# Kernel optimization log

Hardware: AMD Instinct MI355X
Metric: run time of the kernel (lower is better)

The kernel has to match this reference:

```python
import jax, jax.numpy as jnp
import numpy as np

PATCH = 16      # sqrt(n_patches=256)
ALPHA = 10.0
HEADS, DH = 2, 64


def _fourier(coords, Bm):
    # coords: (HW, 2), Bm: (n_features, 2) -> (HW, 2*n_features)
    proj = 2.0 * jnp.pi * coords @ Bm.T
    return jnp.concatenate([jnp.cos(proj), jnp.sin(proj)], axis=-1)


def _forward(coords_decoding, tokens, B_q, B_l0, B_l1,
             qW, qb, toqW, tokvW, tooW, toob,
             bwW0, bwb0, bwW1, bwb1,
             modW0, modb0, modW1, modb1,
             hvW0, hvb0, outW0, outb0, outW1, outb1):
    B = coords_decoding.shape[0]
    Hh, Ww = coords_decoding.shape[1], coords_decoding.shape[2]
    coords = coords_decoding.reshape(B, -1, coords_decoding.shape[-1])
    grid = coords[0]                      # (HW, 2); coords_modulation is None -> same grid
    HW = grid.shape[0]
    m = tokens.shape[1]

    # patch indices and spatial bias
    row = jnp.clip((grid[:, 0] * PATCH).astype(jnp.int32), 0, PATCH - 1)
    col = jnp.clip((grid[:, 1] * PATCH).astype(jnp.int32), 0, PATCH - 1)
    idx = row * PATCH + col               # (HW,)
    t = idx.astype(jnp.float32) / (PATCH * PATCH)
    pos = (jnp.arange(m, dtype=jnp.float32) + 0.5) / m
    rel = -ALPHA * jnp.abs(t[None, :] - pos[:, None]) ** 2   # (m, HW)
    bias = rel.T                          # (HW, m), broadcast over batch & heads

    # query features (shared across batch)
    xq = jax.nn.relu(_fourier(grid, B_q) @ qW + qb)           # (HW, hd)
    xq_b = jnp.broadcast_to(xq[None], (B, HW, xq.shape[-1]))

    # cross attention with spatial bias
    q = (xq_b @ toqW).reshape(B, HW, HEADS, DH).transpose(0, 2, 1, 3)   # (B,h,HW,Dh)
    kv = tokens @ tokvW                                                  # (B,m,2*inner)
    k, v = jnp.split(kv, 2, axis=-1)
    k = k.reshape(B, m, HEADS, DH).transpose(0, 2, 1, 3)                 # (B,h,m,Dh)
    v = v.reshape(B, m, HEADS, DH).transpose(0, 2, 1, 3)
    sim = jnp.einsum('bhqd,bhkd->bhqk', q, k) * (DH ** -0.5) + bias[None, None]
    attn = jax.nn.softmax(sim, axis=-1)
    o = jnp.einsum('bhqk,bhkd->bhqd', attn, v)
    o = o.transpose(0, 2, 1, 3).reshape(B, HW, HEADS * DH)
    mod = o @ tooW + toob                                                # (B,HW,hd)

    # per-band MLP stack (layer_num = 2)
    def band(Bl, bwW, bwb, mW, mb):
        h = jax.nn.relu(_fourier(grid, Bl) @ bwW + bwb)                  # (HW,hd)
        return jax.nn.relu(h[None] + mod @ mW + mb)                      # (B,HW,hd)

    m0 = band(B_l0, bwW0, bwb0, modW0, modb0)
    m1 = band(B_l1, bwW1, bwb1, modW1, modb1)
    hv0 = m0
    hv1 = jax.nn.relu((m1 + hv0) @ hvW0 + hvb0)
    out = (hv0 @ outW0 + outb0) + (hv1 @ outW1 + outb1)                  # (B,HW,3)
    return out.reshape(B, Hh, Ww, -1)


def setup_inputs() -> dict:
    key = jax.random.key(0)
    ks = jax.random.split(key, 32)
    B, H, W, L = 4, 128, 128, 256
    fd, hd, cd, od = 64, 256, 256, 3
    nf = fd // 2
    inner = HEADS * DH

    def lin(k, i, o):
        return jax.random.normal(k, (i, o), dtype=jnp.float32) / np.sqrt(i).astype(np.float32)

    inp = {}
    inp['coords_decoding'] = jax.random.uniform(ks[0], (B, H, W, 2), dtype=jnp.float32)
    inp['tokens'] = jax.random.normal(ks[1], (B, L, cd), dtype=jnp.float32)
    inp['B_q'] = jax.random.normal(ks[2], (nf, 2), dtype=jnp.float32) / 16.0
    inp['B_l0'] = jax.random.normal(ks[3], (nf, 2), dtype=jnp.float32) / 128.0
    inp['B_l1'] = jax.random.normal(ks[4], (nf, 2), dtype=jnp.float32) / 32.0
    inp['qW'] = lin(ks[5], fd, hd); inp['qb'] = jnp.zeros((hd,), jnp.float32)
    inp['toqW'] = lin(ks[6], hd, inner)
    inp['tokvW'] = lin(ks[7], cd, inner * 2)
    inp['tooW'] = lin(ks[8], inner, hd); inp['toob'] = jnp.zeros((hd,), jnp.float32)
    inp['bwW0'] = lin(ks[9], fd, hd); inp['bwb0'] = jnp.zeros((hd,), jnp.float32)
    inp['bwW1'] = lin(ks[10], fd, hd); inp['bwb1'] = jnp.zeros((hd,), jnp.float32)
    inp['modW0'] = lin(ks[11], hd, hd); inp['modb0'] = jnp.zeros((hd,), jnp.float32)
    inp['modW1'] = lin(ks[12], hd, hd); inp['modb1'] = jnp.zeros((hd,), jnp.float32)
    inp['hvW0'] = lin(ks[13], hd, hd); inp['hvb0'] = jnp.zeros((hd,), jnp.float32)
    inp['outW0'] = lin(ks[14], hd, od); inp['outb0'] = jnp.zeros((od,), jnp.float32)
    inp['outW1'] = lin(ks[15], hd, od); inp['outb1'] = jnp.zeros((od,), jnp.float32)
    return inp


def reference(coords_decoding, tokens, B_q, B_l0, B_l1,
              qW, qb, toqW, tokvW, tooW, toob,
              bwW0, bwb0, bwW1, bwb1,
              modW0, modb0, modW1, modb1,
              hvW0, hvb0, outW0, outb0, outW1, outb1):
    return _forward(coords_decoding, tokens, B_q, B_l0, B_l1,
                    qW, qb, toqW, tokvW, tooW, toob,
                    bwW0, bwb0, bwW1, bwb1,
                    modW0, modb0, modW1, modb1,
                    hvW0, hvb0, outW0, outb0, outW1, outb1)
```

## Files before the change

kernel.cpp:

```cpp
#include <hip/hip_runtime.h>
#include <stdint.h>

constexpr int kHW = 16384;
constexpr int kB  = 4;
constexpr int kM  = 256;

typedef _Float16 half8 __attribute__((ext_vector_type(8)));
typedef __attribute__((ext_vector_type(4))) float f32x4;
typedef unsigned int u32x4 __attribute__((ext_vector_type(4)));

__device__ __forceinline__ unsigned short f2h(float f) {
  _Float16 h = (_Float16)f;
  return __builtin_bit_cast(unsigned short, h);
}
__device__ __forceinline__ float h2f(unsigned short u) {
  return (float)__builtin_bit_cast(_Float16, u);
}

__global__ __launch_bounds__(256) void wprep_kernel(
    const float* __restrict__ tooW, const float* __restrict__ modW0,
    const float* __restrict__ modW1, const float* __restrict__ hvW0,
    const float* __restrict__ qW, const float* __restrict__ bwW0,
    const float* __restrict__ bwW1, const float* __restrict__ toqW,
    unsigned short* __restrict__ tooWt, unsigned short* __restrict__ modW0t,
    unsigned short* __restrict__ modW1t, unsigned short* __restrict__ hvW0t,
    unsigned short* __restrict__ qWt, unsigned short* __restrict__ bw0t,
    unsigned short* __restrict__ bw1t, unsigned short* __restrict__ toqWt)
{
  int m = blockIdx.x, tid = threadIdx.x;
  const float* Ws[8] = {tooW, modW0, modW1, hvW0, qW, bwW0, bwW1, toqW};
  unsigned short* Wts[8] = {tooWt, modW0t, modW1t, hvW0t, qWt, bw0t, bw1t, toqWt};
  const int Ks[8] = {128, 256, 256, 256, 64, 64, 64, 256};
  const int Ns[8] = {256, 256, 256, 256, 256, 256, 256, 128};
  const float* W = Ws[m];
  unsigned short* Wt = Wts[m];
  int K = Ks[m], N = Ns[m];
  if (tid < N) {
    for (int kb = 0; kb < K / 8; kb++) {
      unsigned short sv[8];
#pragma unroll
      for (int i = 0; i < 8; i++)
        sv[i] = f2h(W[(kb * 8 + i) * N + tid]);
      *(uint4*)&Wt[tid * K + kb * 8] = *(const uint4*)sv;
    }
  }
}

__global__ __launch_bounds__(256) void kv_kernel(
    const float* __restrict__ tokens, const float* __restrict__ tokvW,
    unsigned short* __restrict__ kn_ws, unsigned short* __restrict__ vt_ws)
{
  __shared__ __align__(16) float tok[256];
  int b = blockIdx.y, j = blockIdx.x, c = threadIdx.x;
  tok[c] = tokens[(b * kM + j) * 256 + c];
  __syncthreads();
  float acc = 0.f;
  for (int i4 = 0; i4 < 64; i4++) {
    float4 t4 = *(const float4*)&tok[i4 * 4];
    acc += t4.x * tokvW[(i4*4+0)*256 + c] + t4.y * tokvW[(i4*4+1)*256 + c]
         + t4.z * tokvW[(i4*4+2)*256 + c] + t4.w * tokvW[(i4*4+3)*256 + c];
  }
  unsigned short hv = f2h(acc);
  if (c < 128) {
    int h = c >> 6, dd = c & 63;
    kn_ws[((size_t)(b*2+h)*256 + j) * 64 + dd] = hv;
  } else {
    int c2 = c - 128;
    int h = c2 >> 6, dd = c2 & 63;
    vt_ws[((size_t)(b*2+h)*64 + dd) * 256 + j] = hv;
  }
}

constexpr int kFPitch = 72;
constexpr int kXPitch = 264;

__global__ __launch_bounds__(256, 2) void feat_kernel(
    const float* __restrict__ coords,
    const float* __restrict__ Bq, const float* __restrict__ Bl0, const float* __restrict__ Bl1,
    const float* __restrict__ qb, const float* __restrict__ bwb0, const float* __restrict__ bwb1,
    const unsigned short* __restrict__ qWt, const unsigned short* __restrict__ bw0t,
    const unsigned short* __restrict__ bw1t, const unsigned short* __restrict__ toqWt,
    float* __restrict__ t_ws, unsigned short* __restrict__ qc_ws,
    unsigned short* __restrict__ h0_hf, unsigned short* __restrict__ h1_hf)
{
  __shared__ __align__(16) unsigned short ff_s[3][32][kFPitch];
  __shared__ __align__(16) unsigned short xq_s[32][kXPitch];
  __shared__ float coords_s[64];

  int tid = threadIdx.x;
  int px0 = blockIdx.x * 32;
  int w = tid >> 6, ln = tid & 63;
  int c = ln & 15, q = ln >> 4;

  if (tid < 64) coords_s[tid] = coords[px0 * 2 + tid];
  __syncthreads();

#pragma unroll
  for (int r = 0; r < 24; r++) {
    int v = r * 256 + tid;
    int mat = v >> 11;
    int p = (v >> 6) & 31;
    int f = v & 63;
    int fr = f & 31;
    const float* Bm = (mat == 0) ? Bq : (mat == 1 ? Bl0 : Bl1);
    float x = coords_s[p * 2 + 0];
    float y = coords_s[p * 2 + 1];
    float proj = 6.283185307179586f * (x * Bm[fr*2+0] + y * Bm[fr*2+1]);
    float s, cc;
    __sincosf(proj, &s, &cc);
    ff_s[mat][p][f] = f2h((f < 32) ? cc : s);
  }
  if (tid < 32) {
    float x = coords_s[tid * 2 + 0];
    float y = coords_s[tid * 2 + 1];
    int row = min(max((int)(x * 16.0f), 0), 15);
    int col = min(max((int)(y * 16.0f), 0), 15);
    t_ws[px0 + tid] = (float)(row * 16 + col) * (1.0f / 256.0f);
  }
  __syncthreads();

  const f32x4 zero4 = {0.f, 0.f, 0.f, 0.f};

  for (int mat = 0; mat < 3; mat++) {
    const unsigned short* Wt = (mat == 0) ? qWt : (mat == 1 ? bw0t : bw1t);
    const float* bias = (mat == 0) ? qb : (mat == 1 ? bwb0 : bwb1);
    f32x4 acc[8];
#pragma unroll
    for (int i = 0; i < 8; i++) acc[i] = zero4;
#pragma unroll
    for (int ks = 0; ks < 2; ks++) {
      int koff = ks * 32 + q * 8;
      half8 bfr[4];
#pragma unroll
      for (int nt = 0; nt < 4; nt++)
        bfr[nt] = *(const half8*)(Wt + (size_t)(w*64 + nt*16 + c) * 64 + koff);
      half8 afr[2];
#pragma unroll
      for (int mt = 0; mt < 2; mt++)
        afr[mt] = *(const half8*)(&ff_s[mat][mt*16 + c][koff]);
#pragma unroll
      for (int mt = 0; mt < 2; mt++)
#pragma unroll
        for (int nt = 0; nt < 4; nt++)
          acc[mt*4+nt] = __builtin_amdgcn_mfma_f32_16x16x32_f16(afr[mt], bfr[nt], acc[mt*4+nt], 0, 0, 0);
    }
    float bv[4];
#pragma unroll
    for (int nt = 0; nt < 4; nt++) bv[nt] = bias[w*64 + nt*16 + c];
#pragma unroll
    for (int mt = 0; mt < 2; mt++)
#pragma unroll
      for (int nt = 0; nt < 4; nt++)
#pragma unroll
        for (int rg = 0; rg < 4; rg++) {
          int row = mt*16 + q*4 + rg, col = w*64 + nt*16 + c;
          unsigned short hv = f2h(fmaxf(acc[mt*4+nt][rg] + bv[nt], 0.f));
          if (mat == 0)      xq_s[row][col] = hv;
          else if (mat == 1) h0_hf[((size_t)(px0 + row)) * 256 + col] = hv;
          else               h1_hf[((size_t)(px0 + row)) * 256 + col] = hv;
        }
  }
  __syncthreads();

  {
    f32x4 acc2[4];
#pragma unroll
    for (int i = 0; i < 4; i++) acc2[i] = zero4;
#pragma unroll
    for (int kt = 0; kt < 8; kt++) {
      int koff = kt * 32 + q * 8;
      half8 bfr[2];
#pragma unroll
      for (int nt = 0; nt < 2; nt++)
        bfr[nt] = *(const half8*)(toqWt + (size_t)(w*32 + nt*16 + c) * 256 + koff);
      half8 afr[2];
#pragma unroll
      for (int mt = 0; mt < 2; mt++)
        afr[mt] = *(const half8*)(&xq_s[mt*16 + c][koff]);
#pragma unroll
      for (int mt = 0; mt < 2; mt++)
#pragma unroll
        for (int nt = 0; nt < 2; nt++)
          acc2[mt*2+nt] = __builtin_amdgcn_mfma_f32_16x16x32_f16(afr[mt], bfr[nt], acc2[mt*2+nt], 0, 0, 0);
    }
#pragma unroll
    for (int mt = 0; mt < 2; mt++)
#pragma unroll
      for (int nt = 0; nt < 2; nt++)
#pragma unroll
        for (int rg = 0; rg < 4; rg++) {
          int row = mt*16 + q*4 + rg, col = w*32 + nt*16 + c;
          qc_ws[((size_t)(px0 + row)) * 128 + col] = f2h(acc2[mt*2+nt][rg]);
        }
  }
}

constexpr int kPPitch = 264;

__global__ __launch_bounds__(256, 2) void attn_kernel(
    const unsigned short* __restrict__ kn_ws,
    const unsigned short* __restrict__ vt_ws,
    const unsigned short* __restrict__ qc_ws,
    const float* __restrict__ t_ws,
    unsigned short* __restrict__ o_hf)
{
  __shared__ __align__(16) unsigned short P_s[32 * kPPitch];
  __shared__ float t_s[32];
  __shared__ float red_max[32][4];
  __shared__ float red_sum[32][4];

  int b = blockIdx.y;
  int px0 = blockIdx.x * 32;
  int tid = threadIdx.x;
  int w = tid >> 6, ln = tid & 63;
  int c = ln & 15, q = ln >> 4;

  if (tid < 32) t_s[tid] = t_ws[px0 + tid];

  const f32x4 zero4 = {0.f, 0.f, 0.f, 0.f};

  for (int h = 0; h < 2; h++) {
    __syncthreads();

    f32x4 acc[8];
#pragma unroll
    for (int i = 0; i < 8; i++) acc[i] = zero4;
    const unsigned short* kbase = kn_ws + (size_t)(b*2+h) * 256 * 64;
#pragma unroll
    for (int ks = 0; ks < 2; ks++) {
      int koff = ks * 32 + q * 8;
      half8 a0 = *(const half8*)(qc_ws + (size_t)(px0 + c) * 128 + h*64 + koff);
      half8 a1 = *(const half8*)(qc_ws + (size_t)(px0 + 16 + c) * 128 + h*64 + koff);
#pragma unroll
      for (int nt = 0; nt < 4; nt++) {
        half8 bf = *(const half8*)(kbase + (size_t)(w*64 + nt*16 + c) * 64 + koff);
        acc[0*4+nt] = __builtin_amdgcn_mfma_f32_16x16x32_f16(a0, bf, acc[0*4+nt], 0, 0, 0);
        acc[1*4+nt] = __builtin_amdgcn_mfma_f32_16x16x32_f16(a1, bf, acc[1*4+nt], 0, 0, 0);
      }
    }

    float lm[2][4];
#pragma unroll
    for (int mt = 0; mt < 2; mt++)
#pragma unroll
      for (int rg = 0; rg < 4; rg++) {
        int row = mt*16 + q*4 + rg;
        float tv = t_s[row];
        float mx = -1e30f;
#pragma unroll
        for (int nt = 0; nt < 4; nt++) {
          int token = w*64 + nt*16 + c;
          float pos = ((float)token + 0.5f) * (1.0f / 256.0f);
          float db = tv - pos;
          float sb = acc[mt*4+nt][rg] * 0.125f - 10.0f * db * db;
          acc[mt*4+nt][rg] = sb;
          mx = fmaxf(mx, sb);
        }
        lm[mt][rg] = mx;
      }
#pragma unroll
    for (int s = 1; s < 16; s <<= 1)
#pragma unroll
      for (int mt = 0; mt < 2; mt++)
#pragma unroll
        for (int rg = 0; rg < 4; rg++)
          lm[mt][rg] = fmaxf(lm[mt][rg], __shfl_xor(lm[mt][rg], s, 64));
    if (c == 0) {
#pragma unroll
      for (int mt = 0; mt < 2; mt++)
#pragma unroll
        for (int rg = 0; rg < 4; rg++)
          red_max[mt*16 + q*4 + rg][w] = lm[mt][rg];
    }
    __syncthreads();

    float ps[2][4];
#pragma unroll
    for (int mt = 0; mt < 2; mt++)
#pragma unroll
      for (int rg = 0; rg < 4; rg++) {
        int row = mt*16 + q*4 + rg;
        float gm = fmaxf(fmaxf(red_max[row][0], red_max[row][1]),
                         fmaxf(red_max[row][2], red_max[row][3]));
        float sum = 0.f;
#pragma unroll
        for (int nt = 0; nt < 4; nt++) {
          float e = __expf(acc[mt*4+nt][rg] - gm);
          sum += e;
          P_s[row * kPPitch + w*64 + nt*16 + c] = f2h(e);
        }
        ps[mt][rg] = sum;
      }
#pragma unroll
    for (int s = 1; s < 16; s <<= 1)
#pragma unroll
      for (int mt = 0; mt < 2; mt++)
#pragma unroll
        for (int rg = 0; rg < 4; rg++)
          ps[mt][rg] += __shfl_xor(ps[mt][rg], s, 64);
    if (c == 0) {
#pragma unroll
      for (int mt = 0; mt < 2; mt++)
#pragma unroll
        for (int rg = 0; rg < 4; rg++)
          red_sum[mt*16 + q*4 + rg][w] = ps[mt][rg];
    }
    __syncthreads();

    f32x4 oacc[2] = {zero4, zero4};
    const unsigned short* vbase = vt_ws + (size_t)(b*2+h) * 64 * 256;
#pragma unroll
    for (int kt = 0; kt < 8; kt++) {
      int koff = kt * 32 + q * 8;
      half8 bf = *(const half8*)(vbase + (size_t)(w*16 + c) * 256 + koff);
      half8 a0 = *(const half8*)(P_s + (0*16 + c) * kPPitch + koff);
      half8 a1 = *(const half8*)(P_s + (1*16 + c) * kPPitch + koff);
      oacc[0] = __builtin_amdgcn_mfma_f32_16x16x32_f16(a0, bf, oacc[0], 0, 0, 0);
      oacc[1] = __builtin_amdgcn_mfma_f32_16x16x32_f16(a1, bf, oacc[1], 0, 0, 0);
    }
#pragma unroll
    for (int mt = 0; mt < 2; mt++)
#pragma unroll
      for (int rg = 0; rg < 4; rg++) {
        int row = mt*16 + q*4 + rg;
        float rinv = 1.0f / (red_sum[row][0] + red_sum[row][1] +
                             red_sum[row][2] + red_sum[row][3]);
        o_hf[((size_t)(b * kHW + px0 + row)) * 128 + h*64 + w*16 + c] =
            f2h(oacc[mt][rg] * rinv);
      }
  }
}

constexpr int kPitch = 264;

template <int KD>
__device__ __forceinline__ void gemm4(
    const unsigned short* abuf, const unsigned short* wt,
    f32x4* acc , int c, int q)
{
  constexpr int NKS = KD / 32;
  const unsigned short* wr0 = wt + (0 * 16 + c) * KD + q * 8;
  const unsigned short* wr1 = wt + (1 * 16 + c) * KD + q * 8;
  const unsigned short* wr2 = wt + (2 * 16 + c) * KD + q * 8;
  const unsigned short* wr3 = wt + (3 * 16 + c) * KD + q * 8;
  half8 bfr[3][4];
#pragma unroll
  for (int p = 0; p < 2; p++) {
    bfr[p][0] = *(const half8*)(wr0 + p * 32);
    bfr[p][1] = *(const half8*)(wr1 + p * 32);
    bfr[p][2] = *(const half8*)(wr2 + p * 32);
    bfr[p][3] = *(const half8*)(wr3 + p * 32);
  }
#pragma unroll
  for (int ks = 0; ks < NKS; ks++) {
    if (ks + 2 < NKS) {
      int slot = (ks + 2) % 3, koff2 = (ks + 2) * 32;
      bfr[slot][0] = *(const half8*)(wr0 + koff2);
      bfr[slot][1] = *(const half8*)(wr1 + koff2);
      bfr[slot][2] = *(const half8*)(wr2 + koff2);
      bfr[slot][3] = *(const half8*)(wr3 + koff2);
    }
    half8 afr[4];
    int koff = ks * 32 + q * 8;
#pragma unroll
    for (int mt = 0; mt < 4; mt++)
      afr[mt] = *(const half8*)(abuf + (mt * 16 + c) * kPitch + koff);
    int cur = ks % 3;
#pragma unroll
    for (int mt = 0; mt < 4; mt++)
#pragma unroll
      for (int nt = 0; nt < 4; nt++)
        acc[mt * 4 + nt] = __builtin_amdgcn_mfma_f32_16x16x32_f16(afr[mt], bfr[cur][nt], acc[mt * 4 + nt], 0, 0, 0);
  }
}

__global__ __launch_bounds__(256, 2) void mlp_kernel(
    const unsigned short* __restrict__ o_hf,
    const unsigned short* __restrict__ h0_hf, const unsigned short* __restrict__ h1_hf,
    const unsigned short* __restrict__ tooWt, const float* __restrict__ toob,
    const unsigned short* __restrict__ modW0t, const float* __restrict__ modb0,
    const unsigned short* __restrict__ modW1t, const float* __restrict__ modb1,
    const unsigned short* __restrict__ hvW0t, const float* __restrict__ hvb0,
    const float* __restrict__ outW0, const float* __restrict__ outb0,
    const float* __restrict__ outW1, const float* __restrict__ outb1,
    float* __restrict__ dout)
{
  __shared__ __align__(16) unsigned short buf0[64 * kPitch];
  __shared__ __align__(16) unsigned short buf1[64 * kPitch];
  __shared__ float scratch[64 * 12];

  int tid = threadIdx.x;
  int px0 = blockIdx.x * 16;
  int w = tid >> 6, ln = tid & 63;
  int c = ln & 15, q = ln >> 4;

  unsigned short h0r[4][4], h1r[4][4];
#pragma unroll
  for (int nt = 0; nt < 4; nt++) {
    int col = w * 64 + nt * 16 + c;
#pragma unroll
    for (int rg = 0; rg < 4; rg++) {
      int px = q * 4 + rg;
      h0r[nt][rg] = __builtin_nontemporal_load(h0_hf + ((size_t)(px0 + px)) * 256 + col);
      h1r[nt][rg] = __builtin_nontemporal_load(h1_hf + ((size_t)(px0 + px)) * 256 + col);
    }
  }

#pragma unroll
  for (int i = 0; i < 4; i++) {
    int idx = i * 256 + tid;
    int r = idx >> 4, c8 = (idx & 15) * 8;
    int b = r >> 4, px = r & 15;
    u32x4 v = __builtin_nontemporal_load(
        (const u32x4*)(o_hf + ((size_t)(b * kHW + px0 + px)) * 128 + c8));
    *(u32x4*)&buf0[r * kPitch + c8] = v;
  }
  __syncthreads();

  const f32x4 zero4 = {0.f, 0.f, 0.f, 0.f};
  f32x4 acc[16];

#pragma unroll
  for (int i = 0; i < 16; i++) acc[i] = zero4;
  gemm4<128>(buf0, tooWt + (size_t)w * 64 * 128, acc, c, q);
  {
    float bias[4];
#pragma unroll
    for (int nt = 0; nt < 4; nt++) bias[nt] = toob[w * 64 + nt * 16 + c];
#pragma unroll
    for (int mt = 0; mt < 4; mt++)
#pragma unroll
      for (int nt = 0; nt < 4; nt++)
#pragma unroll
        for (int rg = 0; rg < 4; rg++) {
          int row = mt * 16 + q * 4 + rg, col = w * 64 + nt * 16 + c;
          buf1[row * kPitch + col] = f2h(acc[mt * 4 + nt][rg] + bias[nt]);
        }
  }
  __syncthreads();

#pragma unroll
  for (int i = 0; i < 16; i++) acc[i] = zero4;
  gemm4<256>(buf1, modW0t + (size_t)w * 64 * 256, acc, c, q);
  {
    float bias[4];
#pragma unroll
    for (int nt = 0; nt < 4; nt++) bias[nt] = modb0[w * 64 + nt * 16 + c];
#pragma unroll
    for (int mt = 0; mt < 4; mt++)
#pragma unroll
      for (int nt = 0; nt < 4; nt++)
#pragma unroll
        for (int rg = 0; rg < 4; rg++) {
          int row = mt * 16 + q * 4 + rg, col = w * 64 + nt * 16 + c;
          buf0[row * kPitch + col] =
              f2h(fmaxf(acc[mt * 4 + nt][rg] + bias[nt] + h2f(h0r[nt][rg]), 0.f));
        }
  }
  __syncthreads();

#pragma unroll
  for (int i = 0; i < 16; i++) acc[i] = zero4;
  gemm4<256>(buf1, modW1t + (size_t)w * 64 * 256, acc, c, q);
  __syncthreads();
  {
    float bias[4];
#pragma unroll
    for (int nt = 0; nt < 4; nt++) bias[nt] = modb1[w * 64 + nt * 16 + c];
#pragma unroll
    for (int mt = 0; mt < 4; mt++)
#pragma unroll
      for (int nt = 0; nt < 4; nt++)
#pragma unroll
        for (int rg = 0; rg < 4; rg++) {
          int row = mt * 16 + q * 4 + rg, col = w * 64 + nt * 16 + c;
          float m0v = h2f(buf0[row * kPitch + col]);
          float v = m0v + fmaxf(acc[mt * 4 + nt][rg] + bias[nt] + h2f(h1r[nt][rg]), 0.f);
          buf1[row * kPitch + col] = f2h(v);
        }
  }
  __syncthreads();

#pragma unroll
  for (int i = 0; i < 16; i++) acc[i] = zero4;
  gemm4<256>(buf1, hvW0t + (size_t)w * 64 * 256, acc, c, q);
  {
    float bias[4], w0v[4][3], w1v[4][3];
#pragma unroll
    for (int nt = 0; nt < 4; nt++) {
      int col = w * 64 + nt * 16 + c;
      bias[nt] = hvb0[col];
#pragma unroll
      for (int k = 0; k < 3; k++) {
        w0v[nt][k] = outW0[col * 3 + k];
        w1v[nt][k] = outW1[col * 3 + k];
      }
    }
#pragma unroll
    for (int mt = 0; mt < 4; mt++) {
      float pk[4][3];
#pragma unroll
      for (int rg = 0; rg < 4; rg++)
#pragma unroll
        for (int k = 0; k < 3; k++) pk[rg][k] = 0.f;
#pragma unroll
      for (int nt = 0; nt < 4; nt++) {
        int col = w * 64 + nt * 16 + c;
#pragma unroll
        for (int rg = 0; rg < 4; rg++) {
          int row = mt * 16 + q * 4 + rg;
          float hv1 = fmaxf(acc[mt * 4 + nt][rg] + bias[nt], 0.f);
          float m0v = h2f(buf0[row * kPitch + col]);
#pragma unroll
          for (int k = 0; k < 3; k++)
            pk[rg][k] += m0v * w0v[nt][k] + hv1 * w1v[nt][k];
        }
      }
#pragma unroll
      for (int s = 1; s < 16; s <<= 1)
#pragma unroll
        for (int rg = 0; rg < 4; rg++)
#pragma unroll
          for (int k = 0; k < 3; k++)
            pk[rg][k] += __shfl_xor(pk[rg][k], s, 64);
      if (c == 0) {
#pragma unroll
        for (int rg = 0; rg < 4; rg++) {
          int row = mt * 16 + q * 4 + rg;
#pragma unroll
          for (int k = 0; k < 3; k++)
            scratch[row * 12 + k * 4 + w] = pk[rg][k];
        }
      }
    }
  }
  __syncthreads();

  if (tid < 192) {
    int row = tid / 3, k = tid % 3;
    int b = row >> 4, px = px0 + (row & 15);
    float s = outb0[k] + outb1[k];
#pragma unroll
    for (int ww = 0; ww < 4; ww++) s += scratch[row * 12 + k * 4 + ww];
    __builtin_nontemporal_store(s, dout + ((size_t)b * kHW + px) * 3 + k);
  }
}

extern "C" void kernel_launch(void* const* d_in, const int* in_sizes, int n_in,
                              void* d_out, int out_size, void* d_ws, size_t ws_size,
                              hipStream_t stream) {
  const float* coords = (const float*)d_in[0];
  const float* tokens = (const float*)d_in[1];
  const float* Bq     = (const float*)d_in[2];
  const float* Bl0    = (const float*)d_in[3];
  const float* Bl1    = (const float*)d_in[4];
  const float* qW     = (const float*)d_in[5];
  const float* qb     = (const float*)d_in[6];
  const float* toqW   = (const float*)d_in[7];
  const float* tokvW  = (const float*)d_in[8];
  const float* tooW   = (const float*)d_in[9];
  const float* toob   = (const float*)d_in[10];
  const float* bwW0   = (const float*)d_in[11];
  const float* bwb0   = (const float*)d_in[12];
  const float* bwW1   = (const float*)d_in[13];
  const float* bwb1   = (const float*)d_in[14];
  const float* modW0  = (const float*)d_in[15];
  const float* modb0  = (const float*)d_in[16];
  const float* modW1  = (const float*)d_in[17];
  const float* modb1  = (const float*)d_in[18];
  const float* hvW0   = (const float*)d_in[19];
  const float* hvb0   = (const float*)d_in[20];
  const float* outW0  = (const float*)d_in[21];
  const float* outb0  = (const float*)d_in[22];
  const float* outW1  = (const float*)d_in[23];
  const float* outb1  = (const float*)d_in[24];

  char* ws = (char*)d_ws;
  float*          t_ws   = (float*)(ws + 0);
  unsigned short* qc_ws  = (unsigned short*)(ws + 65536);
  unsigned short* h0_hf  = (unsigned short*)(ws + 4259840);
  unsigned short* h1_hf  = (unsigned short*)(ws + 12648448);
  unsigned short* o_hf   = (unsigned short*)(ws + 21037056);
  unsigned short* kn_ws  = (unsigned short*)(ws + 37814272);
  unsigned short* vt_ws  = (unsigned short*)(ws + 38076416);
  unsigned short* tooWt  = (unsigned short*)(ws + 38338560);
  unsigned short* modW0t = (unsigned short*)(ws + 38404096);
  unsigned short* modW1t = (unsigned short*)(ws + 38535168);
  unsigned short* hvW0t  = (unsigned short*)(ws + 38666240);
  unsigned short* qWt    = (unsigned short*)(ws + 38797312);
  unsigned short* bw0t   = (unsigned short*)(ws + 38830080);
  unsigned short* bw1t   = (unsigned short*)(ws + 38862848);
  unsigned short* toqWt  = (unsigned short*)(ws + 38895616);

  wprep_kernel<<<dim3(8), 256, 0, stream>>>(
      tooW, modW0, modW1, hvW0, qW, bwW0, bwW1, toqW,
      tooWt, modW0t, modW1t, hvW0t, qWt, bw0t, bw1t, toqWt);
  feat_kernel<<<dim3(kHW / 32), 256, 0, stream>>>(
      coords, Bq, Bl0, Bl1, qb, bwb0, bwb1,
      qWt, bw0t, bw1t, toqWt,
      t_ws, qc_ws, h0_hf, h1_hf);
  kv_kernel<<<dim3(kM, kB), 256, 0, stream>>>(tokens, tokvW, kn_ws, vt_ws);
  attn_kernel<<<dim3(kHW / 32, kB), 256, 0, stream>>>(kn_ws, vt_ws, qc_ws, t_ws, o_hf);
  mlp_kernel<<<dim3(kHW / 16), 256, 0, stream>>>(
      o_hf, h0_hf, h1_hf, tooWt, toob, modW0t, modb0, modW1t, modb1,
      hvW0t, hvb0, outW0, outb0, outW1, outb1, (float*)d_out);
}
```

Before: 260.6 us.

## Fuse feature, attention and MLP kernels into one per-pixel-tile kernel

Merges the Fourier-feature/query projection, the cross-attention and the MLP stack into a single kernel over 16-pixel tiles. Query features, band activations (h0/h1) and attention outputs now stay in registers or LDS instead of going through global workspace buffers. This removes tens of MB of global writes and reads plus two kernel launches. In exchange, the per-tile GEMMs are smaller (16 rows), and the attention loop over batch and heads runs serially inside each block with extra barriers. The gemm4 helper also loses its triple-buffered weight prefetch, and the output store is no longer nontemporal.

```diff
diff --git a/kernel.cpp b/kernel.cpp
--- a/kernel.cpp
+++ b/kernel.cpp
@@ -7,7 +7,6 @@
 
 typedef _Float16 half8 __attribute__((ext_vector_type(8)));
 typedef __attribute__((ext_vector_type(4))) float f32x4;
-typedef unsigned int u32x4 __attribute__((ext_vector_type(4)));
 
 __device__ __forceinline__ unsigned short f2h(float f) {
   _Float16 h = (_Float16)f;
@@ -71,312 +70,40 @@
   }
 }
 
-constexpr int kFPitch = 72;
-constexpr int kXPitch = 264;
-
-__global__ __launch_bounds__(256, 2) void feat_kernel(
+constexpr int kPitch  = 264;
+constexpr int kQPitch = 136;
+
+template <int KD>
+__device__ __forceinline__ void gemm4(
+    const unsigned short* abuf, const unsigned short* wt,
+    f32x4* acc , int c, int q)
+{
+#pragma unroll
+  for (int ks = 0; ks < KD / 32; ks++) {
+    int koff = ks * 32 + q * 8;
+    half8 bfr[4];
+#pragma unroll
+    for (int nt = 0; nt < 4; nt++)
+      bfr[nt] = *(const half8*)(wt + (nt * 16 + c) * KD + koff);
+    half8 afr[4];
+#pragma unroll
+    for (int mt = 0; mt < 4; mt++)
+      afr[mt] = *(const half8*)(abuf + (mt * 16 + c) * kPitch + koff);
+#pragma unroll
+    for (int mt = 0; mt < 4; mt++)
+#pragma unroll
+      for (int nt = 0; nt < 4; nt++)
+        acc[mt * 4 + nt] = __builtin_amdgcn_mfma_f32_16x16x32_f16(afr[mt], bfr[nt], acc[mt * 4 + nt], 0, 0, 0);
+  }
+}
+
+__global__ __launch_bounds__(256, 2) void fused_kernel(
     const float* __restrict__ coords,
     const float* __restrict__ Bq, const float* __restrict__ Bl0, const float* __restrict__ Bl1,
     const float* __restrict__ qb, const float* __restrict__ bwb0, const float* __restrict__ bwb1,
     const unsigned short* __restrict__ qWt, const unsigned short* __restrict__ bw0t,
     const unsigned short* __restrict__ bw1t, const unsigned short* __restrict__ toqWt,
-    float* __restrict__ t_ws, unsigned short* __restrict__ qc_ws,
-    unsigned short* __restrict__ h0_hf, unsigned short* __restrict__ h1_hf)
-{
-  __shared__ __align__(16) unsigned short ff_s[3][32][kFPitch];
-  __shared__ __align__(16) unsigned short xq_s[32][kXPitch];
-  __shared__ float coords_s[64];
-
-  int tid = threadIdx.x;
-  int px0 = blockIdx.x * 32;
-  int w = tid >> 6, ln = tid & 63;
-  int c = ln & 15, q = ln >> 4;
-
-  if (tid < 64) coords_s[tid] = coords[px0 * 2 + tid];
-  __syncthreads();
-
-#pragma unroll
-  for (int r = 0; r < 24; r++) {
-    int v = r * 256 + tid;
-    int mat = v >> 11;
-    int p = (v >> 6) & 31;
-    int f = v & 63;
-    int fr = f & 31;
-    const float* Bm = (mat == 0) ? Bq : (mat == 1 ? Bl0 : Bl1);
-    float x = coords_s[p * 2 + 0];
-    float y = coords_s[p * 2 + 1];
-    float proj = 6.283185307179586f * (x * Bm[fr*2+0] + y * Bm[fr*2+1]);
-    float s, cc;
-    __sincosf(proj, &s, &cc);
-    ff_s[mat][p][f] = f2h((f < 32) ? cc : s);
-  }
-  if (tid < 32) {
-    float x = coords_s[tid * 2 + 0];
-    float y = coords_s[tid * 2 + 1];
-    int row = min(max((int)(x * 16.0f), 0), 15);
-    int col = min(max((int)(y * 16.0f), 0), 15);
-    t_ws[px0 + tid] = (float)(row * 16 + col) * (1.0f / 256.0f);
-  }
-  __syncthreads();
-
-  const f32x4 zero4 = {0.f, 0.f, 0.f, 0.f};
-
-  for (int mat = 0; mat < 3; mat++) {
-    const unsigned short* Wt = (mat == 0) ? qWt : (mat == 1 ? bw0t : bw1t);
-    const float* bias = (mat == 0) ? qb : (mat == 1 ? bwb0 : bwb1);
-    f32x4 acc[8];
-#pragma unroll
-    for (int i = 0; i < 8; i++) acc[i] = zero4;
-#pragma unroll
-    for (int ks = 0; ks < 2; ks++) {
-      int koff = ks * 32 + q * 8;
-      half8 bfr[4];
-#pragma unroll
-      for (int nt = 0; nt < 4; nt++)
-        bfr[nt] = *(const half8*)(Wt + (size_t)(w*64 + nt*16 + c) * 64 + koff);
-      half8 afr[2];
-#pragma unroll
-      for (int mt = 0; mt < 2; mt++)
-        afr[mt] = *(const half8*)(&ff_s[mat][mt*16 + c][koff]);
-#pragma unroll
-      for (int mt = 0; mt < 2; mt++)
-#pragma unroll
-        for (int nt = 0; nt < 4; nt++)
-          acc[mt*4+nt] = __builtin_amdgcn_mfma_f32_16x16x32_f16(afr[mt], bfr[nt], acc[mt*4+nt], 0, 0, 0);
-    }
-    float bv[4];
-#pragma unroll
-    for (int nt = 0; nt < 4; nt++) bv[nt] = bias[w*64 + nt*16 + c];
-#pragma unroll
-    for (int mt = 0; mt < 2; mt++)
-#pragma unroll
-      for (int nt = 0; nt < 4; nt++)
-#pragma unroll
-        for (int rg = 0; rg < 4; rg++) {
-          int row = mt*16 + q*4 + rg, col = w*64 + nt*16 + c;
-          unsigned short hv = f2h(fmaxf(acc[mt*4+nt][rg] + bv[nt], 0.f));
-          if (mat == 0)      xq_s[row][col] = hv;
-          else if (mat == 1) h0_hf[((size_t)(px0 + row)) * 256 + col] = hv;
-          else               h1_hf[((size_t)(px0 + row)) * 256 + col] = hv;
-        }
-  }
-  __syncthreads();
-
-  {
-    f32x4 acc2[4];
-#pragma unroll
-    for (int i = 0; i < 4; i++) acc2[i] = zero4;
-#pragma unroll
-    for (int kt = 0; kt < 8; kt++) {
-      int koff = kt * 32 + q * 8;
-      half8 bfr[2];
-#pragma unroll
-      for (int nt = 0; nt < 2; nt++)
-        bfr[nt] = *(const half8*)(toqWt + (size_t)(w*32 + nt*16 + c) * 256 + koff);
-      half8 afr[2];
-#pragma unroll
-      for (int mt = 0; mt < 2; mt++)
-        afr[mt] = *(const half8*)(&xq_s[mt*16 + c][koff]);
-#pragma unroll
-      for (int mt = 0; mt < 2; mt++)
-#pragma unroll
-        for (int nt = 0; nt < 2; nt++)
-          acc2[mt*2+nt] = __builtin_amdgcn_mfma_f32_16x16x32_f16(afr[mt], bfr[nt], acc2[mt*2+nt], 0, 0, 0);
-    }
-#pragma unroll
-    for (int mt = 0; mt < 2; mt++)
-#pragma unroll
-      for (int nt = 0; nt < 2; nt++)
-#pragma unroll
-        for (int rg = 0; rg < 4; rg++) {
-          int row = mt*16 + q*4 + rg, col = w*32 + nt*16 + c;
-          qc_ws[((size_t)(px0 + row)) * 128 + col] = f2h(acc2[mt*2+nt][rg]);
-        }
-  }
-}
-
-constexpr int kPPitch = 264;
-
-__global__ __launch_bounds__(256, 2) void attn_kernel(
-    const unsigned short* __restrict__ kn_ws,
-    const unsigned short* __restrict__ vt_ws,
-    const unsigned short* __restrict__ qc_ws,
-    const float* __restrict__ t_ws,
-    unsigned short* __restrict__ o_hf)
-{
-  __shared__ __align__(16) unsigned short P_s[32 * kPPitch];
-  __shared__ float t_s[32];
-  __shared__ float red_max[32][4];
-  __shared__ float red_sum[32][4];
-
-  int b = blockIdx.y;
-  int px0 = blockIdx.x * 32;
-  int tid = threadIdx.x;
-  int w = tid >> 6, ln = tid & 63;
-  int c = ln & 15, q = ln >> 4;
-
-  if (tid < 32) t_s[tid] = t_ws[px0 + tid];
-
-  const f32x4 zero4 = {0.f, 0.f, 0.f, 0.f};
-
-  for (int h = 0; h < 2; h++) {
-    __syncthreads();
-
-    f32x4 acc[8];
-#pragma unroll
-    for (int i = 0; i < 8; i++) acc[i] = zero4;
-    const unsigned short* kbase = kn_ws + (size_t)(b*2+h) * 256 * 64;
-#pragma unroll
-    for (int ks = 0; ks < 2; ks++) {
-      int koff = ks * 32 + q * 8;
-      half8 a0 = *(const half8*)(qc_ws + (size_t)(px0 + c) * 128 + h*64 + koff);
-      half8 a1 = *(const half8*)(qc_ws + (size_t)(px0 + 16 + c) * 128 + h*64 + koff);
-#pragma unroll
-      for (int nt = 0; nt < 4; nt++) {
-        half8 bf = *(const half8*)(kbase + (size_t)(w*64 + nt*16 + c) * 64 + koff);
-        acc[0*4+nt] = __builtin_amdgcn_mfma_f32_16x16x32_f16(a0, bf, acc[0*4+nt], 0, 0, 0);
-        acc[1*4+nt] = __builtin_amdgcn_mfma_f32_16x16x32_f16(a1, bf, acc[1*4+nt], 0, 0, 0);
-      }
-    }
-
-    float lm[2][4];
-#pragma unroll
-    for (int mt = 0; mt < 2; mt++)
-#pragma unroll
-      for (int rg = 0; rg < 4; rg++) {
-        int row = mt*16 + q*4 + rg;
-        float tv = t_s[row];
-        float mx = -1e30f;
-#pragma unroll
-        for (int nt = 0; nt < 4; nt++) {
-          int token = w*64 + nt*16 + c;
-          float pos = ((float)token + 0.5f) * (1.0f / 256.0f);
-          float db = tv - pos;
-          float sb = acc[mt*4+nt][rg] * 0.125f - 10.0f * db * db;
-          acc[mt*4+nt][rg] = sb;
-          mx = fmaxf(mx, sb);
-        }
-        lm[mt][rg] = mx;
-      }
-#pragma unroll
-    for (int s = 1; s < 16; s <<= 1)
-#pragma unroll
-      for (int mt = 0; mt < 2; mt++)
-#pragma unroll
-        for (int rg = 0; rg < 4; rg++)
-          lm[mt][rg] = fmaxf(lm[mt][rg], __shfl_xor(lm[mt][rg], s, 64));
-    if (c == 0) {
-#pragma unroll
-      for (int mt = 0; mt < 2; mt++)
-#pragma unroll
-        for (int rg = 0; rg < 4; rg++)
-          red_max[mt*16 + q*4 + rg][w] = lm[mt][rg];
-    }
-    __syncthreads();
-
-    float ps[2][4];
-#pragma unroll
-    for (int mt = 0; mt < 2; mt++)
-#pragma unroll
-      for (int rg = 0; rg < 4; rg++) {
-        int row = mt*16 + q*4 + rg;
-        float gm = fmaxf(fmaxf(red_max[row][0], red_max[row][1]),
-                         fmaxf(red_max[row][2], red_max[row][3]));
-        float sum = 0.f;
-#pragma unroll
-        for (int nt = 0; nt < 4; nt++) {
-          float e = __expf(acc[mt*4+nt][rg] - gm);
-          sum += e;
-          P_s[row * kPPitch + w*64 + nt*16 + c] = f2h(e);
-        }
-        ps[mt][rg] = sum;
-      }
-#pragma unroll
-    for (int s = 1; s < 16; s <<= 1)
-#pragma unroll
-      for (int mt = 0; mt < 2; mt++)
-#pragma unroll
-        for (int rg = 0; rg < 4; rg++)
-          ps[mt][rg] += __shfl_xor(ps[mt][rg], s, 64);
-    if (c == 0) {
-#pragma unroll
-      for (int mt = 0; mt < 2; mt++)
-#pragma unroll
-        for (int rg = 0; rg < 4; rg++)
-          red_sum[mt*16 + q*4 + rg][w] = ps[mt][rg];
-    }
-    __syncthreads();
-
-    f32x4 oacc[2] = {zero4, zero4};
-    const unsigned short* vbase = vt_ws + (size_t)(b*2+h) * 64 * 256;
-#pragma unroll
-    for (int kt = 0; kt < 8; kt++) {
-      int koff = kt * 32 + q * 8;
-      half8 bf = *(const half8*)(vbase + (size_t)(w*16 + c) * 256 + koff);
-      half8 a0 = *(const half8*)(P_s + (0*16 + c) * kPPitch + koff);
-      half8 a1 = *(const half8*)(P_s + (1*16 + c) * kPPitch + koff);
-      oacc[0] = __builtin_amdgcn_mfma_f32_16x16x32_f16(a0, bf, oacc[0], 0, 0, 0);
-      oacc[1] = __builtin_amdgcn_mfma_f32_16x16x32_f16(a1, bf, oacc[1], 0, 0, 0);
-    }
-#pragma unroll
-    for (int mt = 0; mt < 2; mt++)
-#pragma unroll
-      for (int rg = 0; rg < 4; rg++) {
-        int row = mt*16 + q*4 + rg;
-        float rinv = 1.0f / (red_sum[row][0] + red_sum[row][1] +
-                             red_sum[row][2] + red_sum[row][3]);
-        o_hf[((size_t)(b * kHW + px0 + row)) * 128 + h*64 + w*16 + c] =
-            f2h(oacc[mt][rg] * rinv);
-      }
-  }
-}
-
-constexpr int kPitch = 264;
-
-template <int KD>
-__device__ __forceinline__ void gemm4(
-    const unsigned short* abuf, const unsigned short* wt,
-    f32x4* acc , int c, int q)
-{
-  constexpr int NKS = KD / 32;
-  const unsigned short* wr0 = wt + (0 * 16 + c) * KD + q * 8;
-  const unsigned short* wr1 = wt + (1 * 16 + c) * KD + q * 8;
-  const unsigned short* wr2 = wt + (2 * 16 + c) * KD + q * 8;
-  const unsigned short* wr3 = wt + (3 * 16 + c) * KD + q * 8;
-  half8 bfr[3][4];
-#pragma unroll
-  for (int p = 0; p < 2; p++) {
-    bfr[p][0] = *(const half8*)(wr0 + p * 32);
-    bfr[p][1] = *(const half8*)(wr1 + p * 32);
-    bfr[p][2] = *(const half8*)(wr2 + p * 32);
-    bfr[p][3] = *(const half8*)(wr3 + p * 32);
-  }
-#pragma unroll
-  for (int ks = 0; ks < NKS; ks++) {
-    if (ks + 2 < NKS) {
-      int slot = (ks + 2) % 3, koff2 = (ks + 2) * 32;
-      bfr[slot][0] = *(const half8*)(wr0 + koff2);
-      bfr[slot][1] = *(const half8*)(wr1 + koff2);
-      bfr[slot][2] = *(const half8*)(wr2 + koff2);
-      bfr[slot][3] = *(const half8*)(wr3 + koff2);
-    }
-    half8 afr[4];
-    int koff = ks * 32 + q * 8;
-#pragma unroll
-    for (int mt = 0; mt < 4; mt++)
-      afr[mt] = *(const half8*)(abuf + (mt * 16 + c) * kPitch + koff);
-    int cur = ks % 3;
-#pragma unroll
-    for (int mt = 0; mt < 4; mt++)
-#pragma unroll
-      for (int nt = 0; nt < 4; nt++)
-        acc[mt * 4 + nt] = __builtin_amdgcn_mfma_f32_16x16x32_f16(afr[mt], bfr[cur][nt], acc[mt * 4 + nt], 0, 0, 0);
-  }
-}
-
-__global__ __launch_bounds__(256, 2) void mlp_kernel(
-    const unsigned short* __restrict__ o_hf,
-    const unsigned short* __restrict__ h0_hf, const unsigned short* __restrict__ h1_hf,
+    const unsigned short* __restrict__ kn_ws, const unsigned short* __restrict__ vt_ws,
     const unsigned short* __restrict__ tooWt, const float* __restrict__ toob,
     const unsigned short* __restrict__ modW0t, const float* __restrict__ modb0,
     const unsigned short* __restrict__ modW1t, const float* __restrict__ modb1,
@@ -387,6 +114,11 @@
 {
   __shared__ __align__(16) unsigned short buf0[64 * kPitch];
   __shared__ __align__(16) unsigned short buf1[64 * kPitch];
+  __shared__ __align__(16) unsigned short qc_s[16 * kQPitch];
+  __shared__ float red_max[16][4];
+  __shared__ float red_sum[16][4];
+  __shared__ float t_s[16];
+  __shared__ float coords_s[32];
   __shared__ float scratch[64 * 12];
 
   int tid = threadIdx.x;
@@ -394,30 +126,182 @@
   int w = tid >> 6, ln = tid & 63;
   int c = ln & 15, q = ln >> 4;
 
+  const f32x4 zero4 = {0.f, 0.f, 0.f, 0.f};
+
+  if (tid < 32) coords_s[tid] = coords[px0 * 2 + tid];
+  __syncthreads();
+
+  unsigned short* ff = buf1;
+#pragma unroll
+  for (int r = 0; r < 12; r++) {
+    int v = r * 256 + tid;
+    int mat = v >> 10;
+    int p = (v >> 6) & 15;
+    int f = v & 63;
+    int fr = f & 31;
+    const float* Bm = (mat == 0) ? Bq : (mat == 1 ? Bl0 : Bl1);
+    float x = coords_s[p * 2 + 0];
+    float y = coords_s[p * 2 + 1];
+    float proj = 6.283185307179586f * (x * Bm[fr*2+0] + y * Bm[fr*2+1]);
+    float s, cc;
+    __sincosf(proj, &s, &cc);
+    ff[(mat * 16 + p) * 72 + f] = f2h((f < 32) ? cc : s);
+  }
+  if (tid < 16) {
+    float x = coords_s[tid * 2 + 0];
+    float y = coords_s[tid * 2 + 1];
+    int row = min(max((int)(x * 16.0f), 0), 15);
+    int col = min(max((int)(y * 16.0f), 0), 15);
+    t_s[tid] = (float)(row * 16 + col) * (1.0f / 256.0f);
+  }
+  __syncthreads();
+
+  unsigned short* xq = buf0;
   unsigned short h0r[4][4], h1r[4][4];
-#pragma unroll
-  for (int nt = 0; nt < 4; nt++) {
-    int col = w * 64 + nt * 16 + c;
-#pragma unroll
-    for (int rg = 0; rg < 4; rg++) {
-      int px = q * 4 + rg;
-      h0r[nt][rg] = __builtin_nontemporal_load(h0_hf + ((size_t)(px0 + px)) * 256 + col);
-      h1r[nt][rg] = __builtin_nontemporal_load(h1_hf + ((size_t)(px0 + px)) * 256 + col);
-    }
-  }
-
-#pragma unroll
-  for (int i = 0; i < 4; i++) {
-    int idx = i * 256 + tid;
-    int r = idx >> 4, c8 = (idx & 15) * 8;
-    int b = r >> 4, px = r & 15;
-    u32x4 v = __builtin_nontemporal_load(
-        (const u32x4*)(o_hf + ((size_t)(b * kHW + px0 + px)) * 128 + c8));
-    *(u32x4*)&buf0[r * kPitch + c8] = v;
-  }
-  __syncthreads();
-
-  const f32x4 zero4 = {0.f, 0.f, 0.f, 0.f};
+  for (int mat = 0; mat < 3; mat++) {
+    const unsigned short* Wt = (mat == 0) ? qWt : (mat == 1 ? bw0t : bw1t);
+    const float* bias = (mat == 0) ? qb : (mat == 1 ? bwb0 : bwb1);
+    f32x4 acc[4];
+#pragma unroll
+    for (int i = 0; i < 4; i++) acc[i] = zero4;
+#pragma unroll
+    for (int ks = 0; ks < 2; ks++) {
+      int koff = ks * 32 + q * 8;
+      half8 afr = *(const half8*)(ff + (mat * 16 + c) * 72 + koff);
+#pragma unroll
+      for (int nt = 0; nt < 4; nt++) {
+        half8 bfr = *(const half8*)(Wt + (size_t)(w*64 + nt*16 + c) * 64 + koff);
+        acc[nt] = __builtin_amdgcn_mfma_f32_16x16x32_f16(afr, bfr, acc[nt], 0, 0, 0);
+      }
+    }
+#pragma unroll
+    for (int nt = 0; nt < 4; nt++) {
+      float bv = bias[w*64 + nt*16 + c];
+#pragma unroll
+      for (int rg = 0; rg < 4; rg++) {
+        unsigned short hv = f2h(fmaxf(acc[nt][rg] + bv, 0.f));
+        if (mat == 0)      xq[(q*4 + rg) * kPitch + w*64 + nt*16 + c] = hv;
+        else if (mat == 1) h0r[nt][rg] = hv;
+        else               h1r[nt][rg] = hv;
+      }
+    }
+  }
+  __syncthreads();
+
+  {
+    f32x4 acc2[2] = {zero4, zero4};
+#pragma unroll
+    for (int kt = 0; kt < 8; kt++) {
+      int koff = kt * 32 + q * 8;
+      half8 afr = *(const half8*)(xq + c * kPitch + koff);
+#pragma unroll
+      for (int nt = 0; nt < 2; nt++) {
+        half8 bfr = *(const half8*)(toqWt + (size_t)(w*32 + nt*16 + c) * 256 + koff);
+        acc2[nt] = __builtin_amdgcn_mfma_f32_16x16x32_f16(afr, bfr, acc2[nt], 0, 0, 0);
+      }
+    }
+#pragma unroll
+    for (int nt = 0; nt < 2; nt++)
+#pragma unroll
+      for (int rg = 0; rg < 4; rg++)
+        qc_s[(q*4 + rg) * kQPitch + w*32 + nt*16 + c] = f2h(acc2[nt][rg]);
+  }
+  __syncthreads();
+
+  for (int b = 0; b < kB; b++) {
+#pragma unroll
+    for (int h = 0; h < 2; h++) {
+      unsigned short* P_s = buf1 + h * 16 * kPitch;
+
+      f32x4 acc[4];
+#pragma unroll
+      for (int i = 0; i < 4; i++) acc[i] = zero4;
+      const unsigned short* kbase = kn_ws + (size_t)(b*2+h) * 256 * 64;
+#pragma unroll
+      for (int ks = 0; ks < 2; ks++) {
+        int koff = ks * 32 + q * 8;
+        half8 a0 = *(const half8*)(qc_s + c * kQPitch + h*64 + koff);
+#pragma unroll
+        for (int nt = 0; nt < 4; nt++) {
+          half8 bf = *(const half8*)(kbase + (size_t)(w*64 + nt*16 + c) * 64 + koff);
+          acc[nt] = __builtin_amdgcn_mfma_f32_16x16x32_f16(a0, bf, acc[nt], 0, 0, 0);
+        }
+      }
+
+      float lm[4];
+#pragma unroll
+      for (int rg = 0; rg < 4; rg++) {
+        int row = q*4 + rg;
+        float tv = t_s[row];
+        float mx = -1e30f;
+#pragma unroll
+        for (int nt = 0; nt < 4; nt++) {
+          int token = w*64 + nt*16 + c;
+          float pos = ((float)token + 0.5f) * (1.0f / 256.0f);
+          float db = tv - pos;
+          float sb = acc[nt][rg] * 0.125f - 10.0f * db * db;
+          acc[nt][rg] = sb;
+          mx = fmaxf(mx, sb);
+        }
+        lm[rg] = mx;
+      }
+#pragma unroll
+      for (int s = 1; s < 16; s <<= 1)
+#pragma unroll
+        for (int rg = 0; rg < 4; rg++)
+          lm[rg] = fmaxf(lm[rg], __shfl_xor(lm[rg], s, 64));
+      if (c == 0) {
+#pragma unroll
+        for (int rg = 0; rg < 4; rg++) red_max[q*4 + rg][w] = lm[rg];
+      }
+      __syncthreads();
+
+      float ps[4];
+#pragma unroll
+      for (int rg = 0; rg < 4; rg++) {
+        int row = q*4 + rg;
+        float gm = fmaxf(fmaxf(red_max[row][0], red_max[row][1]),
+                         fmaxf(red_max[row][2], red_max[row][3]));
+        float sum = 0.f;
+#pragma unroll
+        for (int nt = 0; nt < 4; nt++) {
+          float e = __expf(acc[nt][rg] - gm);
+          sum += e;
+          P_s[row * kPitch + w*64 + nt*16 + c] = f2h(e);
+        }
+        ps[rg] = sum;
+      }
+#pragma unroll
+      for (int s = 1; s < 16; s <<= 1)
+#pragma unroll
+        for (int rg = 0; rg < 4; rg++)
+          ps[rg] += __shfl_xor(ps[rg], s, 64);
+      if (c == 0) {
+#pragma unroll
+        for (int rg = 0; rg < 4; rg++) red_sum[q*4 + rg][w] = ps[rg];
+      }
+      __syncthreads();
+
+      f32x4 oacc = zero4;
+      const unsigned short* vbase = vt_ws + (size_t)(b*2+h) * 64 * 256;
+#pragma unroll
+      for (int kt = 0; kt < 8; kt++) {
+        int koff = kt * 32 + q * 8;
+        half8 bf = *(const half8*)(vbase + (size_t)(w*16 + c) * 256 + koff);
+        half8 a0 = *(const half8*)(P_s + c * kPitch + koff);
+        oacc = __builtin_amdgcn_mfma_f32_16x16x32_f16(a0, bf, oacc, 0, 0, 0);
+      }
+#pragma unroll
+      for (int rg = 0; rg < 4; rg++) {
+        int row = q*4 + rg;
+        float rinv = 1.0f / (red_sum[row][0] + red_sum[row][1] +
+                             red_sum[row][2] + red_sum[row][3]);
+        buf0[(b*16 + row) * kPitch + h*64 + w*16 + c] = f2h(oacc[rg] * rinv);
+      }
+    }
+  }
+  __syncthreads();
+
   f32x4 acc[16];
 
 #pragma unroll
@@ -542,7 +426,7 @@
     float s = outb0[k] + outb1[k];
 #pragma unroll
     for (int ww = 0; ww < 4; ww++) s += scratch[row * 12 + k * 4 + ww];
-    __builtin_nontemporal_store(s, dout + ((size_t)b * kHW + px) * 3 + k);
+    dout[((size_t)b * kHW + px) * 3 + k] = s;
   }
 }
 
@@ -576,32 +460,25 @@
   const float* outb1  = (const float*)d_in[24];
 
   char* ws = (char*)d_ws;
-  float*          t_ws   = (float*)(ws + 0);
-  unsigned short* qc_ws  = (unsigned short*)(ws + 65536);
-  unsigned short* h0_hf  = (unsigned short*)(ws + 4259840);
-  unsigned short* h1_hf  = (unsigned short*)(ws + 12648448);
-  unsigned short* o_hf   = (unsigned short*)(ws + 21037056);
-  unsigned short* kn_ws  = (unsigned short*)(ws + 37814272);
-  unsigned short* vt_ws  = (unsigned short*)(ws + 38076416);
-  unsigned short* tooWt  = (unsigned short*)(ws + 38338560);
-  unsigned short* modW0t = (unsigned short*)(ws + 38404096);
-  unsigned short* modW1t = (unsigned short*)(ws + 38535168);
-  unsigned short* hvW0t  = (unsigned short*)(ws + 38666240);
-  unsigned short* qWt    = (unsigned short*)(ws + 38797312);
-  unsigned short* bw0t   = (unsigned short*)(ws + 38830080);
-  unsigned short* bw1t   = (unsigned short*)(ws + 38862848);
-  unsigned short* toqWt  = (unsigned short*)(ws + 38895616);
+  unsigned short* kn_ws  = (unsigned short*)(ws + 0);
+  unsigned short* vt_ws  = (unsigned short*)(ws + 262144);
+  unsigned short* tooWt  = (unsigned short*)(ws + 524288);
+  unsigned short* modW0t = (unsigned short*)(ws + 589824);
+  unsigned short* modW1t = (unsigned short*)(ws + 720896);
+  unsigned short* hvW0t  = (unsigned short*)(ws + 851968);
+  unsigned short* qWt    = (unsigned short*)(ws + 983040);
+  unsigned short* bw0t   = (unsigned short*)(ws + 1015808);
+  unsigned short* bw1t   = (unsigned short*)(ws + 1048576);
+  unsigned short* toqWt  = (unsigned short*)(ws + 1081344);
 
   wprep_kernel<<<dim3(8), 256, 0, stream>>>(
       tooW, modW0, modW1, hvW0, qW, bwW0, bwW1, toqW,
       tooWt, modW0t, modW1t, hvW0t, qWt, bw0t, bw1t, toqWt);
-  feat_kernel<<<dim3(kHW / 32), 256, 0, stream>>>(
+  kv_kernel<<<dim3(kM, kB), 256, 0, stream>>>(tokens, tokvW, kn_ws, vt_ws);
+  fused_kernel<<<dim3(kHW / 16), 256, 0, stream>>>(
       coords, Bq, Bl0, Bl1, qb, bwb0, bwb1,
       qWt, bw0t, bw1t, toqWt,
-      t_ws, qc_ws, h0_hf, h1_hf);
-  kv_kernel<<<dim3(kM, kB), 256, 0, stream>>>(tokens, tokvW, kn_ws, vt_ws);
-  attn_kernel<<<dim3(kHW / 32, kB), 256, 0, stream>>>(kn_ws, vt_ws, qc_ws, t_ws, o_hf);
-  mlp_kernel<<<dim3(kHW / 16), 256, 0, stream>>>(
-      o_hf, h0_hf, h1_hf, tooWt, toob, modW0t, modb0, modW1t, modb1,
+      kn_ws, vt_ws,
+      tooWt, toob, modW0t, modb0, modW1t, modb1,
       hvW0t, hvb0, outW0, outb0, outW1, outb1, (float*)d_out);
 }
```

New measurement: 277.7 us. 1.07x slower.
